# Performance work log

Hardware: AMD Instinct MI355X
Metric: run time of the kernel (lower is better)

Reference implementation:

```python
import jax, jax.numpy as jnp
import numpy as np

N_NODES = 100_000
N_EDGES = 1_600_000
N_GRAPHS = 2048
IN_CH, HID, EMB = 6, 64, 16
N_LIG, N_ADD, N_BASE, N_ARYL = 12, 23, 4, 16
TOTAL_IN = HID + 4 * EMB  # 128


def setup_inputs() -> dict:
    key = jax.random.key(0)
    ks = jax.random.split(key, 20)
    p = lambda k, shape: (jax.random.normal(k, shape, jnp.float32) * 0.05)
    return {
        "x": jax.random.normal(ks[0], (N_NODES, IN_CH), jnp.float32),
        "edge_index": jax.random.randint(ks[1], (2, N_EDGES), 0, N_NODES),
        "batch": jnp.sort(jax.random.randint(ks[2], (N_NODES,), 0, N_GRAPHS)),
        "ligand_idx": jax.random.randint(ks[3], (N_GRAPHS,), 0, N_LIG),
        "additive_idx": jax.random.randint(ks[4], (N_GRAPHS,), 0, N_ADD),
        "base_idx": jax.random.randint(ks[5], (N_GRAPHS,), 0, N_BASE),
        "aryl_idx": jax.random.randint(ks[6], (N_GRAPHS,), 0, N_ARYL),
        "emb_ligand": p(ks[7], (N_LIG, EMB)),
        "emb_additive": p(ks[8], (N_ADD, EMB)),
        "emb_base": p(ks[9], (N_BASE, EMB)),
        "emb_aryl": p(ks[10], (N_ARYL, EMB)),
        "W1": p(ks[11], (IN_CH, HID)),
        "b1": jnp.zeros((HID,), jnp.float32),
        "W2": p(ks[12], (HID, HID)),
        "b2": jnp.zeros((HID,), jnp.float32),
        "lin1_W": p(ks[13], (TOTAL_IN, HID)),
        "lin1_b": jnp.zeros((HID,), jnp.float32),
        "lin2_W": p(ks[14], (HID, 1)),
        "lin2_b": jnp.zeros((1,), jnp.float32),
    }


def gcn_conv(x, src, dst, W, b):
    """PyG GCNConv: add self-loops, sym-normalize, aggregate xW over edges."""
    n = x.shape[0]
    xw = x @ W  # [N, out]
    loop = jnp.arange(n)
    s = jnp.concatenate([src, loop])
    d = jnp.concatenate([dst, loop])
    deg = jax.ops.segment_sum(jnp.ones_like(d, dtype=xw.dtype), d, num_segments=n)
    dinv = jax.lax.rsqrt(jnp.maximum(deg, 1.0))  # deg >= 1 due to self-loops
    norm = (dinv[s] * dinv[d])[:, None]
    return jax.ops.segment_sum(xw[s] * norm, d, num_segments=n) + b


def reference(x, edge_index, batch, ligand_idx, additive_idx, base_idx, aryl_idx,
              emb_ligand, emb_additive, emb_base, emb_aryl,
              W1, b1, W2, b2, lin1_W, lin1_b, lin2_W, lin2_b):
    src, dst = edge_index[0], edge_index[1]
    h = jax.nn.relu(gcn_conv(x, src, dst, W1, b1))
    h = jax.nn.relu(gcn_conv(h, src, dst, W2, b2))
    # global mean pool over graphs
    sums = jax.ops.segment_sum(h, batch, num_segments=N_GRAPHS)
    cnt = jax.ops.segment_sum(jnp.ones((h.shape[0],), h.dtype), batch, num_segments=N_GRAPHS)
    pooled = sums / jnp.maximum(cnt, 1.0)[:, None]  # [G, HID]
    cat = jnp.concatenate([
        pooled,
        emb_ligand[ligand_idx], emb_additive[additive_idx],
        emb_base[base_idx], emb_aryl[aryl_idx],
    ], axis=-1)  # [G, HID + 4*EMB]
    hmid = jax.nn.relu(cat @ lin1_W + lin1_b)  # dropout is identity in eval mode
    return hmid @ lin2_W + lin2_b  # [G, 1]
```

## Files before the change

### kernel.cpp

```cpp
#include <hip/hip_runtime.h>
#include <hip/hip_bf16.h>

#define PCHUNK 4096
#define NBK 1024
#define BSZ 128
#define CAP 2560
#define CNT_STRIDE 16

__device__ inline float bf2f(unsigned int u16) { return __uint_as_float(u16 << 16); }
__device__ inline unsigned short f2bf(float f) {
    __hip_bfloat16 b = __float2bfloat16(f);
    return *(unsigned short*)&b;
}

typedef __attribute__((ext_vector_type(8))) short v8s;
typedef __attribute__((ext_vector_type(4))) float v4f;

__global__ void k_partition(const int* __restrict__ src, const int* __restrict__ dst, int E,
                            int* __restrict__ bucket_cnt, unsigned int* __restrict__ buckets,
                            float* __restrict__ zero_base, int zero_count) {
    __shared__ int hist[NBK];
    __shared__ int shift[NBK];
    __shared__ int cursor[NBK];
    __shared__ unsigned int staged_e[PCHUNK];
    __shared__ unsigned short staged_b[PCHUNK];
    __shared__ int wtot[4];
    int t = threadIdx.x;
    int lane = t & 63, wave = t >> 6;
    int base = blockIdx.x * PCHUNK;
    for (int i = blockIdx.x * 256 + t; i < zero_count; i += gridDim.x * 256)
        zero_base[i] = 0.f;
    for (int i = t; i < NBK; i += 256) hist[i] = 0;
    __syncthreads();
    int nE = E - base; if (nE > PCHUNK) nE = PCHUNK;
    for (int i = t; i < nE; i += 256) atomicAdd(&hist[dst[base + i] >> 7], 1);
    __syncthreads();
    int h0 = hist[4 * t], h1 = hist[4 * t + 1], h2 = hist[4 * t + 2], h3 = hist[4 * t + 3];
    int p1 = h0 + h1, p2 = p1 + h2, s = p2 + h3;
    int si = s;
    #pragma unroll
    for (int off = 1; off < 64; off <<= 1) {
        int u = __shfl_up(si, off, 64);
        if (lane >= off) si += u;
    }
    if (lane == 63) wtot[wave] = si;
    __syncthreads();
    int woff = 0;
    #pragma unroll
    for (int w2 = 0; w2 < 4; ++w2) woff += (w2 < wave) ? wtot[w2] : 0;
    int ebase = woff + si - s;
    int ex[4] = {ebase, ebase + h0, ebase + p1, ebase + p2};
    int cn[4] = {h0, h1, h2, h3};
    #pragma unroll
    for (int j = 0; j < 4; ++j) {
        int bidx = 4 * t + j;
        cursor[bidx] = ex[j];
        if (cn[j] > 0) {
            int g = atomicAdd(&bucket_cnt[bidx * CNT_STRIDE], cn[j]);
            shift[bidx] = g - ex[j];
        }
    }
    __syncthreads();
    for (int i = t; i < nE; i += 256) {
        int d = dst[base + i];
        int b = d >> 7;
        int r = atomicAdd(&cursor[b], 1);
        staged_e[r] = (unsigned int)src[base + i] | ((unsigned int)(d & (BSZ - 1)) << 24);
        staged_b[r] = (unsigned short)b;
    }
    __syncthreads();
    for (int i = t; i < nE; i += 256) {
        int b = staged_b[i];
        buckets[(size_t)b * CAP + shift[b] + i] = staged_e[i];
    }
}

__global__ void k_bucket_csr_xd(const unsigned int* __restrict__ buckets,
                                const int* __restrict__ bucket_cnt,
                                int* __restrict__ offs, int* __restrict__ deg,
                                float* __restrict__ dinv, int* __restrict__ csr,
                                const float* __restrict__ x,
                                float* __restrict__ xd, int N) {
    __shared__ int dl[BSZ], cur[BSZ];
    __shared__ float dis[BSZ];
    __shared__ float xs[BSZ * 6];
    __shared__ int w0tot;
    int b = blockIdx.x, t = threadIdx.x;
    int nb0 = b * BSZ;
    for (int i = t; i < BSZ * 6; i += 256) {
        int node = nb0 + i / 6;
        xs[i] = (node < N) ? x[(size_t)nb0 * 6 + i] : 0.f;
    }
    if (t < BSZ) dl[t] = 0;
    __syncthreads();
    int cnt = bucket_cnt[b * CNT_STRIDE];
    if (cnt > CAP) cnt = CAP;
    const unsigned int* bp = buckets + (size_t)b * CAP;
    for (int i = t; i < cnt; i += 256) atomicAdd(&dl[bp[i] >> 24], 1);
    __syncthreads();
    int lane = t & 63, wave = t >> 6;
    int v = (t < BSZ) ? dl[t] : 0;
    int si = v;
    #pragma unroll
    for (int off = 1; off < 64; off <<= 1) {
        int u = __shfl_up(si, off, 64);
        if (lane >= off) si += u;
    }
    if (t == 63) w0tot = si;
    __syncthreads();
    int ex = si - v + ((wave == 1) ? w0tot : 0);
    if (t < BSZ) {
        cur[t] = ex;
        float di = rsqrtf((float)v + 1.0f);
        dis[t] = di;
        int n = nb0 + t;
        if (n < N) { offs[n] = b * CAP + ex; deg[n] = v; dinv[n] = di; }
    }
    __syncthreads();
    int* cg = csr + (size_t)b * CAP;
    for (int i = t; i < cnt; i += 256) {
        unsigned int e = bp[i];
        int r = atomicAdd(&cur[e >> 24], 1);
        cg[r] = (int)(e & 0x00FFFFFFu);
    }
    #pragma unroll
    for (int j = 0; j < 4; ++j) {
        int idx = t + j * 256;
        int nl = idx >> 3, c = idx & 7;
        int node = nb0 + nl;
        if (node < N)
            xd[((size_t)node << 3) + c] = (c < 6) ? xs[nl * 6 + c] * dis[nl] : 0.f;
    }
}

__global__ void k_pull1_xw2(const float* __restrict__ xd, const int* __restrict__ csr,
                            const int* __restrict__ offs, const int* __restrict__ deg,
                            const float* __restrict__ dinv,
                            const float* __restrict__ W1, const float* __restrict__ b1,
                            const float* __restrict__ W2, unsigned short* __restrict__ A2,
                            int N) {
    __shared__ float agg6[32][8];
    __shared__ unsigned short Ht[32][72];
    __shared__ float W1s[6 * 64];
    int t = threadIdx.x;
    int lane = t & 63, wave = t >> 6;
    int q = lane >> 4, m16 = lane & 15;
    int cbase = wave * 16;
    for (int i = t; i < 6 * 64; i += 256) W1s[i] = W1[i];
    v8s b0h, b0l, b1h, b1l;
    #pragma unroll
    for (int j = 0; j < 8; ++j) {
        float w0 = W2[(q * 8 + j) * 64 + cbase + m16];
        unsigned short h0 = f2bf(w0);
        b0h[j] = (short)h0;
        b0l[j] = (short)f2bf(w0 - bf2f(h0));
        float w1 = W2[(32 + q * 8 + j) * 64 + cbase + m16];
        unsigned short h1 = f2bf(w1);
        b1h[j] = (short)h1;
        b1l[j] = (short)f2bf(w1 - bf2f(h1));
    }
    int n0 = blockIdx.x * 32;
    int oct = lane >> 3, m = lane & 7;
    int nl = wave * 8 + oct;
    int n = n0 + nl;
    bool valid = n < N;
    int nc = valid ? n : N - 1;
    int base = offs[nc];
    int dg = valid ? deg[nc] : 0;
    int dgm = dg, o;
    o = __shfl_xor(dgm, 8, 64);  dgm = dgm > o ? dgm : o;
    o = __shfl_xor(dgm, 16, 64); dgm = dgm > o ? dgm : o;
    o = __shfl_xor(dgm, 32, 64); dgm = dgm > o ? dgm : o;
    float a = xd[((size_t)nc << 3) + m];
    int i = 0;
    for (; i + 8 <= dgm; i += 8) {
        float u[8];
        #pragma unroll
        for (int j = 0; j < 8; ++j) {
            unsigned int s = (unsigned int)csr[base + i + j];
            if (s >= (unsigned int)N) s = 0;
            u[j] = xd[((size_t)s << 3) + m];
        }
        #pragma unroll
        for (int j = 0; j < 8; ++j)
            a += (i + j < dg) ? u[j] : 0.f;
    }
    for (; i < dgm; ++i) {
        unsigned int s = (unsigned int)csr[base + i];
        if (s >= (unsigned int)N) s = 0;
        float u = xd[((size_t)s << 3) + m];
        a += (i < dg) ? u : 0.f;
    }
    agg6[nl][m] = (valid ? dinv[n] : 0.f) * a;
    __syncthreads();
    float bl = b1[lane];
    #pragma unroll
    for (int r = 0; r < 8; ++r) {
        int node_l = wave * 8 + r;
        float acc = bl;
        #pragma unroll
        for (int k = 0; k < 6; ++k) acc += agg6[node_l][k] * W1s[k * 64 + lane];
        Ht[node_l][lane] = f2bf(fmaxf(acc, 0.f));
    }
    __syncthreads();
    #pragma unroll
    for (int tile = 0; tile < 2; ++tile) {
        int row = tile * 16 + m16;
        union { uint4 u; v8s s; } a0u, a1u;
        a0u.u = *(const uint4*)&Ht[row][q * 8];
        a1u.u = *(const uint4*)&Ht[row][32 + q * 8];
        v4f acc = {0.f, 0.f, 0.f, 0.f};
        acc = __builtin_amdgcn_mfma_f32_16x16x32_bf16(a0u.s, b0l, acc, 0, 0, 0);
        acc = __builtin_amdgcn_mfma_f32_16x16x32_bf16(a1u.s, b1l, acc, 0, 0, 0);
        acc = __builtin_amdgcn_mfma_f32_16x16x32_bf16(a0u.s, b0h, acc, 0, 0, 0);
        acc = __builtin_amdgcn_mfma_f32_16x16x32_bf16(a1u.s, b1h, acc, 0, 0, 0);
        #pragma unroll
        for (int r = 0; r < 4; ++r) {
            int node = n0 + tile * 16 + q * 4 + r;
            if (node < N)
                A2[(size_t)node * 64 + cbase + m16] = f2bf(acc[r] * dinv[node]);
        }
    }
}

__global__ void k_pull_pool(const unsigned short* __restrict__ A, const int* __restrict__ csr,
                            const int* __restrict__ offs, const int* __restrict__ deg,
                            const float* __restrict__ dinv, const float* __restrict__ bias,
                            const int* __restrict__ batch, float* __restrict__ pool, int N) {
    __shared__ float vt[4][4][64];
    int t = threadIdx.x;
    int lane = t & 63, wave = t >> 6;
    int q = lane >> 4, m = lane & 15;
    int n0 = blockIdx.x * 16;
    int nl = wave * 4 + q;
    int n = n0 + nl;
    bool valid = n < N;
    int nc = valid ? n : N - 1;
    int base = offs[nc];
    int dg = valid ? deg[nc] : 0;
    int dgm = dg, o;
    o = __shfl_xor(dgm, 16, 64); dgm = dgm > o ? dgm : o;
    o = __shfl_xor(dgm, 32, 64); dgm = dgm > o ? dgm : o;
    uint2 su = *(const uint2*)(A + ((size_t)nc << 6) + 4 * m);
    float a0 = __uint_as_float(su.x << 16);
    float a1 = __uint_as_float(su.x & 0xffff0000u);
    float a2 = __uint_as_float(su.y << 16);
    float a3 = __uint_as_float(su.y & 0xffff0000u);
    int i = 0;
    for (; i + 8 <= dgm; i += 8) {
        uint2 u[8];
        #pragma unroll
        for (int j = 0; j < 8; ++j) {
            unsigned int s = (unsigned int)csr[base + i + j];
            if (s >= (unsigned int)N) s = 0;
            u[j] = *(const uint2*)(A + ((size_t)s << 6) + 4 * m);
        }
        #pragma unroll
        for (int j = 0; j < 8; ++j) {
            unsigned int ux = (i + j < dg) ? u[j].x : 0u;
            unsigned int uy = (i + j < dg) ? u[j].y : 0u;
            a0 += __uint_as_float(ux << 16);
            a1 += __uint_as_float(ux & 0xffff0000u);
            a2 += __uint_as_float(uy << 16);
            a3 += __uint_as_float(uy & 0xffff0000u);
        }
    }
    for (; i < dgm; ++i) {
        unsigned int s = (unsigned int)csr[base + i];
        if (s >= (unsigned int)N) s = 0;
        uint2 uu = *(const uint2*)(A + ((size_t)s << 6) + 4 * m);
        unsigned int ux = (i < dg) ? uu.x : 0u;
        unsigned int uy = (i < dg) ? uu.y : 0u;
        a0 += __uint_as_float(ux << 16);
        a1 += __uint_as_float(ux & 0xffff0000u);
        a2 += __uint_as_float(uy << 16);
        a3 += __uint_as_float(uy & 0xffff0000u);
    }
    float di = valid ? dinv[n] : 0.f;
    float4 bb = *(const float4*)(bias + 4 * m);
    float4 vv;
    vv.x = fmaxf(fmaf(di, a0, bb.x), 0.f);
    vv.y = fmaxf(fmaf(di, a1, bb.y), 0.f);
    vv.z = fmaxf(fmaf(di, a2, bb.z), 0.f);
    vv.w = fmaxf(fmaf(di, a3, bb.w), 0.f);
    *(float4*)&vt[wave][q][4 * m] = vv;
    __syncthreads();
    int nw0 = n0 + wave * 4;
    #pragma unroll
    for (int r = 0; r < 4; ++r) {
        int nn = nw0 + r;
        if (nn < N) {
            float v = vt[wave][r][lane];
            atomicAdd(&pool[(size_t)batch[nn] * 64 + lane], v);
        }
    }
}

__global__ void k_final4(const float* __restrict__ pool, const int* __restrict__ batch,
                         int N, int G,
                         const int* __restrict__ lig, const int* __restrict__ add,
                         const int* __restrict__ base, const int* __restrict__ aryl,
                         const float* __restrict__ e_lig, const float* __restrict__ e_add,
                         const float* __restrict__ e_base, const float* __restrict__ e_aryl,
                         const float* __restrict__ lin1W, const float* __restrict__ lin1b,
                         const float* __restrict__ lin2W, const float* __restrict__ lin2b,
                         float* __restrict__ out) {
    __shared__ float Wl[128 * 64];
    __shared__ float cat[4][128];
    int t = threadIdx.x;
    int c = t & 63, wv = t >> 6;
    for (int i = t; i < 128 * 64; i += 256) Wl[i] = lin1W[i];
    int g = blockIdx.x * 4 + wv;
    if (g < G) {
        int res = 0;
        if (c < 2) {
            int target = g + c;
            int lo = 0, hi = N;
            while (lo < hi) {
                int mid = (lo + hi) >> 1;
                if (batch[mid] < target) lo = mid + 1; else hi = mid;
            }
            res = lo;
        }
        int lo = __shfl(res, 0, 64), hi = __shfl(res, 1, 64);
        float invc = 1.0f / fmaxf((float)(hi - lo), 1.0f);
        cat[wv][c] = pool[(size_t)g * 64 + c] * invc;
        float ev;
        if (c < 16)      ev = e_lig[lig[g] * 16 + c];
        else if (c < 32) ev = e_add[add[g] * 16 + (c - 16)];
        else if (c < 48) ev = e_base[base[g] * 16 + (c - 32)];
        else             ev = e_aryl[aryl[g] * 16 + (c - 48)];
        cat[wv][64 + c] = ev;
    }
    __syncthreads();
    if (g < G) {
        float acc = lin1b[c];
        #pragma unroll
        for (int k = 0; k < 128; ++k) acc += cat[wv][k] * Wl[k * 64 + c];
        float p = fmaxf(acc, 0.f) * lin2W[c];
        #pragma unroll
        for (int off = 32; off > 0; off >>= 1) p += __shfl_down(p, off, 64);
        if (c == 0) out[g] = p + lin2b[0];
    }
}

extern "C" void kernel_launch(void* const* d_in, const int* in_sizes, int n_in,
                              void* d_out, int out_size, void* d_ws, size_t ws_size,
                              hipStream_t stream) {
    const float* x      = (const float*)d_in[0];
    const int*   ei     = (const int*)d_in[1];
    const int*   batch  = (const int*)d_in[2];
    const int*   lig    = (const int*)d_in[3];
    const int*   addi   = (const int*)d_in[4];
    const int*   basei  = (const int*)d_in[5];
    const int*   aryl   = (const int*)d_in[6];
    const float* e_lig  = (const float*)d_in[7];
    const float* e_add  = (const float*)d_in[8];
    const float* e_base = (const float*)d_in[9];
    const float* e_aryl = (const float*)d_in[10];
    const float* W1     = (const float*)d_in[11];
    const float* b1     = (const float*)d_in[12];
    const float* W2     = (const float*)d_in[13];
    const float* b2     = (const float*)d_in[14];
    const float* lin1W  = (const float*)d_in[15];
    const float* lin1b  = (const float*)d_in[16];
    const float* lin2W  = (const float*)d_in[17];
    const float* lin2b  = (const float*)d_in[18];
    float* out = (float*)d_out;

    const int N = in_sizes[0] / 6;
    const int E = in_sizes[1] / 2;
    const int G = in_sizes[3];
    const int* src = ei;
    const int* dst = ei + E;
    const int NBb = (N + BSZ - 1) / BSZ;

    char* w = (char*)d_ws;
    size_t SA = (size_t)N * 64;
    float* xd = (float*)w;     w += (size_t)N * 8 * 4;
    unsigned short* A2 = (unsigned short*)w;  w += SA * 2;
    float* dinv = (float*)w;   w += (size_t)N * 4;
    int*   deg  = (int*)w;     w += (size_t)N * 4;
    int*   offs = (int*)w;     w += (size_t)N * 4;
    float* pool = (float*)w;   w += (size_t)G * 64 * 4;
    int* bucket_cnt = (int*)w; w += (size_t)NBK * CNT_STRIDE * 4;
    unsigned int* buckets = (unsigned int*)w;  w += (size_t)NBb * CAP * 4;
    int* csr    = (int*)w;     w += (size_t)NBb * CAP * 4;
    w += 4096;

    hipMemsetAsync(bucket_cnt, 0, (size_t)NBK * CNT_STRIDE * 4, stream);

    const int npart = (E + PCHUNK - 1) / PCHUNK;
    k_partition<<<npart, 256, 0, stream>>>(src, dst, E, bucket_cnt, buckets,
                                           pool, G * 64);
    k_bucket_csr_xd<<<NBb, 256, 0, stream>>>(buckets, bucket_cnt,
                                             offs, deg, dinv, csr, x, xd, N);

    k_pull1_xw2<<<(N + 31) / 32, 256, 0, stream>>>(xd, csr, offs, deg, dinv,
                                                   W1, b1, W2, A2, N);

    k_pull_pool<<<(N + 15) / 16, 256, 0, stream>>>(A2, csr, offs, deg, dinv, b2, batch, pool, N);

    k_final4<<<(G + 3) / 4, 256, 0, stream>>>(pool, batch, N, G, lig, addi, basei, aryl,
                                              e_lig, e_add, e_base, e_aryl,
                                              lin1W, lin1b, lin2W, lin2b, out);
}
```

Before: 222.4 us.

## Sort nodes by degree within each bucket to balance pull-kernel wavefronts

Builds a per-bucket permutation of nodes, ordered by in-degree through a shared-memory counting sort, inside the CSR construction kernel. Both pull kernels then walk nodes in this permuted order, so the lanes in a wavefront handle nodes of similar degree. This is meant to cut the divergence that comes from looping to the maximum degree in the group. In exchange it adds an indirection load per node, scattered writes to A2 and the pool atomics, and less locality in the per-node arrays.

Result: slower. 236.4 us (+6.3%).

```diff
diff --git a/kernel.cpp b/kernel.cpp
--- a/kernel.cpp
+++ b/kernel.cpp
@@ -80,11 +80,12 @@
                                 int* __restrict__ offs, int* __restrict__ deg,
                                 float* __restrict__ dinv, int* __restrict__ csr,
                                 const float* __restrict__ x,
-                                float* __restrict__ xd, int N) {
+                                float* __restrict__ xd, int* __restrict__ perm, int N) {
     __shared__ int dl[BSZ], cur[BSZ];
     __shared__ float dis[BSZ];
     __shared__ float xs[BSZ * 6];
     __shared__ int w0tot;
+    __shared__ int bin[64];
     int b = blockIdx.x, t = threadIdx.x;
     int nb0 = b * BSZ;
     for (int i = t; i < BSZ * 6; i += 256) {
@@ -92,6 +93,7 @@
         xs[i] = (node < N) ? x[(size_t)nb0 * 6 + i] : 0.f;
     }
     if (t < BSZ) dl[t] = 0;
+    if (t < 64) bin[t] = 0;
     __syncthreads();
     int cnt = bucket_cnt[b * CNT_STRIDE];
     if (cnt > CAP) cnt = CAP;
@@ -109,12 +111,12 @@
     if (t == 63) w0tot = si;
     __syncthreads();
     int ex = si - v + ((wave == 1) ? w0tot : 0);
+    int node_t = nb0 + t;
     if (t < BSZ) {
         cur[t] = ex;
         float di = rsqrtf((float)v + 1.0f);
         dis[t] = di;
-        int n = nb0 + t;
-        if (n < N) { offs[n] = b * CAP + ex; deg[n] = v; dinv[n] = di; }
+        if (node_t < N) { offs[node_t] = b * CAP + ex; deg[node_t] = v; dinv[node_t] = di; }
     }
     __syncthreads();
     int* cg = csr + (size_t)b * CAP;
@@ -131,11 +133,28 @@
         if (node < N)
             xd[((size_t)node << 3) + c] = (c < 6) ? xs[nl * 6 + c] * dis[nl] : 0.f;
     }
+    if (t < BSZ && node_t < N) atomicAdd(&bin[v < 63 ? v : 63], 1);
+    __syncthreads();
+    if (t < 64) {
+        int bv = bin[t], bs = bv;
+        #pragma unroll
+        for (int off = 1; off < 64; off <<= 1) {
+            int u = __shfl_up(bs, off, 64);
+            if (lane >= off) bs += u;
+        }
+        bin[t] = bs - bv;
+    }
+    __syncthreads();
+    if (t < BSZ && node_t < N) {
+        int d = v < 63 ? v : 63;
+        int r = atomicAdd(&bin[d], 1);
+        perm[nb0 + r] = node_t;
+    }
 }
 
 __global__ void k_pull1_xw2(const float* __restrict__ xd, const int* __restrict__ csr,
                             const int* __restrict__ offs, const int* __restrict__ deg,
-                            const float* __restrict__ dinv,
+                            const float* __restrict__ dinv, const int* __restrict__ perm,
                             const float* __restrict__ W1, const float* __restrict__ b1,
                             const float* __restrict__ W2, unsigned short* __restrict__ A2,
                             int N) {
@@ -162,9 +181,9 @@
     int n0 = blockIdx.x * 32;
     int oct = lane >> 3, m = lane & 7;
     int nl = wave * 8 + oct;
-    int n = n0 + nl;
-    bool valid = n < N;
-    int nc = valid ? n : N - 1;
+    int idx = n0 + nl;
+    bool valid = idx < N;
+    int nc = valid ? perm[idx] : 0;
     int base = offs[nc];
     int dg = valid ? deg[nc] : 0;
     int dgm = dg, o;
@@ -191,7 +210,7 @@
         float u = xd[((size_t)s << 3) + m];
         a += (i < dg) ? u : 0.f;
     }
-    agg6[nl][m] = (valid ? dinv[n] : 0.f) * a;
+    agg6[nl][m] = (valid ? dinv[nc] : 0.f) * a;
     __syncthreads();
     float bl = b1[lane];
     #pragma unroll
@@ -216,16 +235,19 @@
         acc = __builtin_amdgcn_mfma_f32_16x16x32_bf16(a1u.s, b1h, acc, 0, 0, 0);
         #pragma unroll
         for (int r = 0; r < 4; ++r) {
-            int node = n0 + tile * 16 + q * 4 + r;
-            if (node < N)
+            int idxs = n0 + tile * 16 + q * 4 + r;
+            if (idxs < N) {
+                int node = perm[idxs];
                 A2[(size_t)node * 64 + cbase + m16] = f2bf(acc[r] * dinv[node]);
+            }
         }
     }
 }
 
 __global__ void k_pull_pool(const unsigned short* __restrict__ A, const int* __restrict__ csr,
                             const int* __restrict__ offs, const int* __restrict__ deg,
-                            const float* __restrict__ dinv, const float* __restrict__ bias,
+                            const float* __restrict__ dinv, const int* __restrict__ perm,
+                            const float* __restrict__ bias,
                             const int* __restrict__ batch, float* __restrict__ pool, int N) {
     __shared__ float vt[4][4][64];
     int t = threadIdx.x;
@@ -233,9 +255,9 @@
     int q = lane >> 4, m = lane & 15;
     int n0 = blockIdx.x * 16;
     int nl = wave * 4 + q;
-    int n = n0 + nl;
-    bool valid = n < N;
-    int nc = valid ? n : N - 1;
+    int idx = n0 + nl;
+    bool valid = idx < N;
+    int nc = valid ? perm[idx] : 0;
     int base = offs[nc];
     int dg = valid ? deg[nc] : 0;
     int dgm = dg, o;
@@ -276,7 +298,7 @@
         a2 += __uint_as_float(uy << 16);
         a3 += __uint_as_float(uy & 0xffff0000u);
     }
-    float di = valid ? dinv[n] : 0.f;
+    float di = valid ? dinv[nc] : 0.f;
     float4 bb = *(const float4*)(bias + 4 * m);
     float4 vv;
     vv.x = fmaxf(fmaf(di, a0, bb.x), 0.f);
@@ -285,11 +307,12 @@
     vv.w = fmaxf(fmaf(di, a3, bb.w), 0.f);
     *(float4*)&vt[wave][q][4 * m] = vv;
     __syncthreads();
-    int nw0 = n0 + wave * 4;
+    int iw0 = n0 + wave * 4;
     #pragma unroll
     for (int r = 0; r < 4; ++r) {
-        int nn = nw0 + r;
-        if (nn < N) {
+        int idxr = iw0 + r;
+        if (idxr < N) {
+            int nn = perm[idxr];
             float v = vt[wave][r][lane];
             atomicAdd(&pool[(size_t)batch[nn] * 64 + lane], v);
         }
@@ -382,6 +405,7 @@
     float* dinv = (float*)w;   w += (size_t)N * 4;
     int*   deg  = (int*)w;     w += (size_t)N * 4;
     int*   offs = (int*)w;     w += (size_t)N * 4;
+    int*   perm = (int*)w;     w += (size_t)NBb * BSZ * 4;
     float* pool = (float*)w;   w += (size_t)G * 64 * 4;
     int* bucket_cnt = (int*)w; w += (size_t)NBK * CNT_STRIDE * 4;
     unsigned int* buckets = (unsigned int*)w;  w += (size_t)NBb * CAP * 4;
@@ -394,12 +418,13 @@
     k_partition<<<npart, 256, 0, stream>>>(src, dst, E, bucket_cnt, buckets,
                                            pool, G * 64);
     k_bucket_csr_xd<<<NBb, 256, 0, stream>>>(buckets, bucket_cnt,
-                                             offs, deg, dinv, csr, x, xd, N);
-
-    k_pull1_xw2<<<(N + 31) / 32, 256, 0, stream>>>(xd, csr, offs, deg, dinv,
+                                             offs, deg, dinv, csr, x, xd, perm, N);
+
+    k_pull1_xw2<<<(N + 31) / 32, 256, 0, stream>>>(xd, csr, offs, deg, dinv, perm,
                                                    W1, b1, W2, A2, N);
 
-    k_pull_pool<<<(N + 15) / 16, 256, 0, stream>>>(A2, csr, offs, deg, dinv, b2, batch, pool, N);
+    k_pull_pool<<<(N + 15) / 16, 256, 0, stream>>>(A2, csr, offs, deg, dinv, perm,
+                                                   b2, batch, pool, N);
 
     k_final4<<<(G + 3) / 4, 256, 0, stream>>>(pool, batch, N, G, lig, addi, basei, aryl,
                                               e_lig, e_add, e_base, e_aryl,
```
